# Optimization experiments

Measured on AMD Instinct MI355X. Metric: run time of the kernel, lower is better.

The kernel has to match this reference:

```python
import jax, jax.numpy as jnp
import numpy as np

B, H, S, D = 2, 12, 3456, 32
FEATS_PER_T = 216
WINDOW_LEN = 8
ACT_SIZE = 16
IMG_FEAT_SIZE = 196
DECODER_ONLY = False


def eye_mask(seq_len, feats_per_t, window_len, act_size, img_feat_size, decoder_only=False):
    """Boolean [S, S] mask replicating get_eye_block_mask's memory_mask."""
    idx = jnp.arange(seq_len)
    q_t = (idx // feats_per_t)[:, None]          # [S,1]
    kv_t = (idx // feats_per_t)[None, :]         # [1,S]
    q_m = (idx % feats_per_t)[:, None]
    kv_m = (idx % feats_per_t)[None, :]
    proprio_idx_mod = 2 + 1 + 1
    img_start = feats_per_t - img_feat_size
    joint_start = img_start - act_size

    causal = (q_t >= kv_t) & (q_t - kv_t < window_len)
    is_q_img = q_m >= img_start
    is_kv_img = kv_m >= img_start
    is_q_joint = (q_m >= joint_start) & (q_m < img_start)
    is_kv_joint = (kv_m >= joint_start) & (kv_m < img_start)
    is_kv_proprio = kv_m == proprio_idx_mod

    img_to_img = ~(is_q_img & is_kv_img)
    same_t = q_t == kv_t
    joint_past_joint = ~(is_q_joint & is_kv_joint & ~same_t)
    proprio_past = ~(is_kv_proprio & (kv_t < q_t))
    past_image = ~(is_kv_img & (kv_t < q_t))
    m = causal & img_to_img & joint_past_joint & proprio_past & past_image
    if decoder_only:
        m = m & ~(is_q_img & ~is_kv_img)
    return m


def setup_inputs() -> dict:
    key = jax.random.key(0)
    kq, kk, kv = jax.random.split(key, 3)
    return {
        "q": jax.random.normal(kq, (B, H, S, D), dtype=jnp.float32),
        "k": jax.random.normal(kk, (B, H, S, D), dtype=jnp.float32),
        "v": jax.random.normal(kv, (B, H, S, D), dtype=jnp.float32),
        "feats_per_t": FEATS_PER_T,
        "window_len": WINDOW_LEN,
        "act_size": ACT_SIZE,
        "img_feat_size": IMG_FEAT_SIZE,
    }


def reference(q, k, v, feats_per_t, window_len, act_size, img_feat_size):
    seq_len = q.shape[2]
    mask = eye_mask(seq_len, feats_per_t, window_len, act_size,
                    img_feat_size, DECODER_ONLY)  # [S,S]
    scale = 1.0 / jnp.sqrt(jnp.array(q.shape[-1], q.dtype))
    scores = jnp.einsum("bhqd,bhkd->bhqk", q, k) * scale
    neg = jnp.asarray(jnp.finfo(scores.dtype).min, scores.dtype)
    scores = jnp.where(mask[None, None], scores, neg)
    attn = jax.nn.softmax(scores, axis=-1)
    return jnp.einsum("bhqk,bhkd->bhqd", attn, v)
```

## Files before the change

### kernel.cpp

```cpp
#include <hip/hip_runtime.h>

#define SEQ   3456
#define DH    32
#define FPT   216
#define NT    16
#define IMG0  20
#define SCALE2 0.25503486f

#define KPAD   40
#define VPAD   168
#define PPITCH 36

typedef __attribute__((ext_vector_type(8))) short bf16x8;
typedef __attribute__((ext_vector_type(4))) short bf16x4;
typedef __attribute__((ext_vector_type(4))) float f32x4;

#define MFMA16(a,b,c) __builtin_amdgcn_mfma_f32_16x16x32_bf16(a,b,c,0,0,0)

__device__ __forceinline__ unsigned short bfh(float f) {
    unsigned u = __float_as_uint(f);
    u += 0x7FFFu + ((u >> 16) & 1u);
    return (unsigned short)(u >> 16);
}
__device__ __forceinline__ float bff(unsigned short h) {
    return __uint_as_float((unsigned)h << 16);
}
__device__ __forceinline__ void split8(const float* f, bf16x8& hi, bf16x8& lo) {
    #pragma unroll
    for (int j = 0; j < 8; ++j) {
        unsigned short h = bfh(f[j]);
        hi[j] = (short)h;
        lo[j] = (short)bfh(f[j] - bff(h));
    }
}
__device__ __forceinline__ bf16x8 load_p(const unsigned short* p) {
    const bf16x4 a = *(const bf16x4*)(p);
    const bf16x4 b = *(const bf16x4*)(p + 4);
    bf16x8 r;
    #pragma unroll
    for (int j = 0; j < 4; ++j) { r[j] = a[j]; r[4 + j] = b[j]; }
    return r;
}

__global__ __launch_bounds__(256, 4)
void eye_attn_mfma2(const float* __restrict__ q, const float* __restrict__ k,
                    const float* __restrict__ v, float* __restrict__ out) {
    __shared__ __align__(16) unsigned short KsHi[160 * KPAD];
    __shared__ __align__(16) unsigned short KsLo[160 * KPAD];
    __shared__ __align__(16) unsigned short VtHi[DH * VPAD];
    __shared__ __align__(16) unsigned short Pu[4 * 16 * PPITCH];

    const int t = blockIdx.x, bh = blockIdx.y, half = blockIdx.z;
    const int tid = threadIdx.x;
    const size_t base = (size_t)bh * SEQ * DH;
    const int dmax = (t < 7) ? t : 7;
    const int nkeys = IMG0 * (dmax + 1);

    for (int i = tid; i < 160 * 8; i += 256) {
        const int g = i >> 3, c = i & 7;
        float4 kk = make_float4(0.f,0.f,0.f,0.f), vv = make_float4(0.f,0.f,0.f,0.f);
        if (g < nkeys) {
            const int d = g / IMG0, jj = g - d * IMG0;
            const size_t row = base + (size_t)((t - d) * FPT + jj) * DH + c * 4;
            kk = *(const float4*)(k + row);
            vv = *(const float4*)(v + row);
        }
        const float kf[4] = {kk.x, kk.y, kk.z, kk.w};
        const float vf[4] = {vv.x, vv.y, vv.z, vv.w};
        ushort4 khi, klo;
        unsigned short* ah = (unsigned short*)&khi;
        unsigned short* al = (unsigned short*)&klo;
        #pragma unroll
        for (int e = 0; e < 4; ++e) {
            const unsigned short h = bfh(kf[e]);
            ah[e] = h;
            al[e] = bfh(kf[e] - bff(h));
        }
        *(ushort4*)(KsHi + g * KPAD + c * 4) = khi;
        *(ushort4*)(KsLo + g * KPAD + c * 4) = klo;
        #pragma unroll
        for (int e = 0; e < 4; ++e)
            VtHi[(c * 4 + e) * VPAD + g] = bfh(vf[e]);
    }
    __syncthreads();

    const int wv = tid >> 6, lane = tid & 63;
    const int col = lane & 15, quad = lane >> 4;

    int mt[2]; int mcnt; bool do_img = false;
    if (half == 0) {
        if (wv == 0)      { mt[0] = 0; mcnt = 1; do_img = true; }
        else if (wv == 1) { mt[0] = 1; mcnt = 1; do_img = true; }
        else if (wv == 2) { mt[0] = 2; mt[1] = 3; mcnt = 2; }
        else              { mt[0] = 4; mt[1] = 5; mcnt = 2; }
    } else {
        mt[0] = 6 + 2 * wv; mt[1] = 7 + 2 * wv; mcnt = 2;
    }

    bf16x8 bones;
    #pragma unroll
    for (int j = 0; j < 8; ++j) bones[j] = (short)(col == 0 ? 0x3F80 : 0);

    unsigned short* myP = Pu + wv * 16 * PPITCH;
    const int nkt = (nkeys + 31) >> 5;

    for (int mi = 0; mi < mcnt; ++mi) {
        const int mb = mt[mi] * 16;
        bf16x8 qhi, qlo;
        {
            const int qc = min(mb + col, FPT - 1);
            const float* qp = q + base + (size_t)(t * FPT + qc) * DH + quad * 8;
            float qf[8];
            const float4 a0 = *(const float4*)qp;
            const float4 a1 = *(const float4*)(qp + 4);
            qf[0]=a0.x*SCALE2; qf[1]=a0.y*SCALE2; qf[2]=a0.z*SCALE2; qf[3]=a0.w*SCALE2;
            qf[4]=a1.x*SCALE2; qf[5]=a1.y*SCALE2; qf[6]=a1.z*SCALE2; qf[7]=a1.w*SCALE2;
            split8(qf, qhi, qlo);
        }
        f32x4 oacc0 = {0.f,0.f,0.f,0.f}, oacc1 = {0.f,0.f,0.f,0.f};
        f32x4 lacc = {0.f,0.f,0.f,0.f};

        for (int kt = 0; kt < nkt; ++kt) {
            f32x4 s[2];
            #pragma unroll
            for (int h = 0; h < 2; ++h) {
                const int key = kt * 32 + h * 16 + col;
                const bf16x8 khi = *(const bf16x8*)(KsHi + key * KPAD + quad * 8);
                const bf16x8 klo = *(const bf16x8*)(KsLo + key * KPAD + quad * 8);
                f32x4 acc = {0.f,0.f,0.f,0.f};
                acc = MFMA16(qhi, khi, acc);
                acc = MFMA16(qlo, khi, acc);
                acc = MFMA16(qhi, klo, acc);
                s[h] = acc;
            }
            #pragma unroll
            for (int h = 0; h < 2; ++h) {
                const int g = kt * 32 + h * 16 + col;
                const int d = g / IMG0, jj = g - d * IMG0;
                #pragma unroll
                for (int r = 0; r < 4; ++r) {
                    const int qm = mb + quad * 4 + r;
                    const bool qj = (qm >= 4) && (qm < IMG0);
                    const bool vis = (g < nkeys) && (qm < FPT) &&
                                     ((d == 0) || ((jj != 4) && !(qj && jj >= 4)));
                    const float e = vis ? __builtin_amdgcn_exp2f(s[h][r]) : 0.f;
                    myP[(quad * 4 + r) * PPITCH + h * 16 + col] = bfh(e);
                }
            }
            const bf16x8 phi = load_p(myP + col * PPITCH + quad * 8);
            #pragma unroll
            for (int h = 0; h < 2; ++h) {
                const int dim = h * 16 + col;
                const bf16x8 vhi = *(const bf16x8*)(VtHi + dim * VPAD + kt * 32 + quad * 8);
                f32x4& oa = h ? oacc1 : oacc0;
                oa = MFMA16(phi, vhi, oa);
            }
            lacc = MFMA16(phi, bones, lacc);
        }

        if (mi == 0 && do_img) {
            for (int kt2 = 0; kt2 < 7; ++kt2) {
                f32x4 s[2];
                #pragma unroll
                for (int h = 0; h < 2; ++h) {
                    const int keyc = min(IMG0 + kt2 * 32 + h * 16 + col, FPT - 1);
                    const float* kp = k + base + (size_t)(t * FPT + keyc) * DH + quad * 8;
                    float kf[8];
                    const float4 a0 = *(const float4*)kp;
                    const float4 a1 = *(const float4*)(kp + 4);
                    kf[0]=a0.x; kf[1]=a0.y; kf[2]=a0.z; kf[3]=a0.w;
                    kf[4]=a1.x; kf[5]=a1.y; kf[6]=a1.z; kf[7]=a1.w;
                    bf16x8 khi, klo;
                    split8(kf, khi, klo);
                    f32x4 acc = {0.f,0.f,0.f,0.f};
                    acc = MFMA16(qhi, khi, acc);
                    acc = MFMA16(qlo, khi, acc);
                    acc = MFMA16(qhi, klo, acc);
                    s[h] = acc;
                }
                #pragma unroll
                for (int h = 0; h < 2; ++h) {
                    const int key = IMG0 + kt2 * 32 + h * 16 + col;
                    #pragma unroll
                    for (int r = 0; r < 4; ++r) {
                        const int qm = mb + quad * 4 + r;
                        const bool vis = (key < FPT) && (qm < IMG0);
                        const float e = vis ? __builtin_amdgcn_exp2f(s[h][r]) : 0.f;
                        myP[(quad * 4 + r) * PPITCH + h * 16 + col] = bfh(e);
                    }
                }
                const bf16x8 phi = load_p(myP + col * PPITCH + quad * 8);
                #pragma unroll
                for (int h = 0; h < 2; ++h) {
                    const int dim = h * 16 + col;
                    float vf[8];
                    #pragma unroll
                    for (int j = 0; j < 8; ++j) {
                        const int ky = min(IMG0 + kt2 * 32 + quad * 8 + j, FPT - 1);
                        vf[j] = v[base + (size_t)(t * FPT + ky) * DH + dim];
                    }
                    bf16x8 vhi;
                    #pragma unroll
                    for (int j = 0; j < 8; ++j) vhi[j] = (short)bfh(vf[j]);
                    f32x4& oa = h ? oacc1 : oacc0;
                    oa = MFMA16(phi, vhi, oa);
                }
                lacc = MFMA16(phi, bones, lacc);
            }
        }

        #pragma unroll
        for (int r = 0; r < 4; ++r) {
            const float lr = __shfl(lacc[r], lane & 48);
            const float inv = 1.f / lr;
            const int qm = mb + quad * 4 + r;
            if (qm < FPT) {
                float* op = out + base + (size_t)(t * FPT + qm) * DH;
                op[col]      = oacc0[r] * inv;
                op[16 + col] = oacc1[r] * inv;
            }
        }
    }
}

extern "C" void kernel_launch(void* const* d_in, const int* in_sizes, int n_in,
                              void* d_out, int out_size, void* d_ws, size_t ws_size,
                              hipStream_t stream) {
    const float* q = (const float*)d_in[0];
    const float* k = (const float*)d_in[1];
    const float* v = (const float*)d_in[2];
    float* out = (float*)d_out;
    const int BH = in_sizes[0] / (SEQ * DH);
    dim3 grid(NT, BH, 2);
    eye_attn_mfma2<<<grid, 256, 0, stream>>>(q, k, v, out);
}
```

Measured before the change: 97.11 us.

## Compute transposed scores so P stays in registers as MFMA B operand

Swaps the MFMA operand order so the score tile is produced transposed (keys along rows, queries along columns). Each lane's exp'd probabilities can then feed the P·V MFMA directly as the B operand, which removes the per-wave LDS round-trip for P and its shared buffer. The V tile is read with two 64-bit LDS loads in the matching permuted key order, and VPAD changes. The row sum now uses an all-ones A operand, and the output is written as float4 vectors without a shuffle.

```diff
diff --git a/kernel.cpp b/kernel.cpp
--- a/kernel.cpp
+++ b/kernel.cpp
@@ -8,8 +8,7 @@
 #define SCALE2 0.25503486f
 
 #define KPAD   40
-#define VPAD   168
-#define PPITCH 36
+#define VPAD   164
 
 typedef __attribute__((ext_vector_type(8))) short bf16x8;
 typedef __attribute__((ext_vector_type(4))) short bf16x4;
@@ -33,9 +32,9 @@
         lo[j] = (short)bfh(f[j] - bff(h));
     }
 }
-__device__ __forceinline__ bf16x8 load_p(const unsigned short* p) {
-    const bf16x4 a = *(const bf16x4*)(p);
-    const bf16x4 b = *(const bf16x4*)(p + 4);
+__device__ __forceinline__ bf16x8 ld2x64(const unsigned short* p0, const unsigned short* p1) {
+    const bf16x4 a = *(const bf16x4*)p0;
+    const bf16x4 b = *(const bf16x4*)p1;
     bf16x8 r;
     #pragma unroll
     for (int j = 0; j < 4; ++j) { r[j] = a[j]; r[4 + j] = b[j]; }
@@ -43,12 +42,11 @@
 }
 
 __global__ __launch_bounds__(256, 4)
-void eye_attn_mfma2(const float* __restrict__ q, const float* __restrict__ k,
+void eye_attn_mfma3(const float* __restrict__ q, const float* __restrict__ k,
                     const float* __restrict__ v, float* __restrict__ out) {
     __shared__ __align__(16) unsigned short KsHi[160 * KPAD];
     __shared__ __align__(16) unsigned short KsLo[160 * KPAD];
     __shared__ __align__(16) unsigned short VtHi[DH * VPAD];
-    __shared__ __align__(16) unsigned short Pu[4 * 16 * PPITCH];
 
     const int t = blockIdx.x, bh = blockIdx.y, half = blockIdx.z;
     const int tid = threadIdx.x;
@@ -97,18 +95,21 @@
         mt[0] = 6 + 2 * wv; mt[1] = 7 + 2 * wv; mcnt = 2;
     }
 
-    bf16x8 bones;
+    bf16x8 ones8;
     #pragma unroll
-    for (int j = 0; j < 8; ++j) bones[j] = (short)(col == 0 ? 0x3F80 : 0);
-
-    unsigned short* myP = Pu + wv * 16 * PPITCH;
+    for (int j = 0; j < 8; ++j) ones8[j] = (short)0x3F80;
+
     const int nkt = (nkeys + 31) >> 5;
+    const int gq = quad * 4;
 
     for (int mi = 0; mi < mcnt; ++mi) {
         const int mb = mt[mi] * 16;
+        const int qm = mb + col;
+        const bool qok = qm < FPT;
+        const bool qj  = (qm >= 4) && (qm < IMG0);
         bf16x8 qhi, qlo;
         {
-            const int qc = min(mb + col, FPT - 1);
+            const int qc = min(qm, FPT - 1);
             const float* qp = q + base + (size_t)(t * FPT + qc) * DH + quad * 8;
             float qf[8];
             const float4 a0 = *(const float4*)qp;
@@ -128,34 +129,32 @@
                 const bf16x8 khi = *(const bf16x8*)(KsHi + key * KPAD + quad * 8);
                 const bf16x8 klo = *(const bf16x8*)(KsLo + key * KPAD + quad * 8);
                 f32x4 acc = {0.f,0.f,0.f,0.f};
-                acc = MFMA16(qhi, khi, acc);
-                acc = MFMA16(qlo, khi, acc);
-                acc = MFMA16(qhi, klo, acc);
+                acc = MFMA16(khi, qhi, acc);
+                acc = MFMA16(khi, qlo, acc);
+                acc = MFMA16(klo, qhi, acc);
                 s[h] = acc;
             }
+            bf16x8 pb;
             #pragma unroll
             for (int h = 0; h < 2; ++h) {
-                const int g = kt * 32 + h * 16 + col;
-                const int d = g / IMG0, jj = g - d * IMG0;
                 #pragma unroll
                 for (int r = 0; r < 4; ++r) {
-                    const int qm = mb + quad * 4 + r;
-                    const bool qj = (qm >= 4) && (qm < IMG0);
-                    const bool vis = (g < nkeys) && (qm < FPT) &&
+                    const int g = kt * 32 + h * 16 + gq + r;
+                    const int d = g / IMG0, jj = g - d * IMG0;
+                    const bool vis = (g < nkeys) && qok &&
                                      ((d == 0) || ((jj != 4) && !(qj && jj >= 4)));
                     const float e = vis ? __builtin_amdgcn_exp2f(s[h][r]) : 0.f;
-                    myP[(quad * 4 + r) * PPITCH + h * 16 + col] = bfh(e);
-                }
-            }
-            const bf16x8 phi = load_p(myP + col * PPITCH + quad * 8);
+                    pb[h * 4 + r] = (short)bfh(e);
+                }
+            }
+            lacc = MFMA16(ones8, pb, lacc);
             #pragma unroll
-            for (int h = 0; h < 2; ++h) {
-                const int dim = h * 16 + col;
-                const bf16x8 vhi = *(const bf16x8*)(VtHi + dim * VPAD + kt * 32 + quad * 8);
-                f32x4& oa = h ? oacc1 : oacc0;
-                oa = MFMA16(phi, vhi, oa);
-            }
-            lacc = MFMA16(phi, bones, lacc);
+            for (int h2 = 0; h2 < 2; ++h2) {
+                const unsigned short* vp = VtHi + (h2 * 16 + col) * VPAD + kt * 32 + quad * 4;
+                const bf16x8 va = ld2x64(vp, vp + 16);
+                f32x4& oa = h2 ? oacc1 : oacc0;
+                oa = MFMA16(va, pb, oa);
+            }
         }
 
         if (mi == 0 && do_img) {
@@ -173,52 +172,48 @@
                     bf16x8 khi, klo;
                     split8(kf, khi, klo);
                     f32x4 acc = {0.f,0.f,0.f,0.f};
-                    acc = MFMA16(qhi, khi, acc);
-                    acc = MFMA16(qlo, khi, acc);
-                    acc = MFMA16(qhi, klo, acc);
+                    acc = MFMA16(khi, qhi, acc);
+                    acc = MFMA16(khi, qlo, acc);
+                    acc = MFMA16(klo, qhi, acc);
                     s[h] = acc;
                 }
+                bf16x8 pb;
                 #pragma unroll
                 for (int h = 0; h < 2; ++h) {
-                    const int key = IMG0 + kt2 * 32 + h * 16 + col;
                     #pragma unroll
                     for (int r = 0; r < 4; ++r) {
-                        const int qm = mb + quad * 4 + r;
+                        const int key = IMG0 + kt2 * 32 + h * 16 + gq + r;
                         const bool vis = (key < FPT) && (qm < IMG0);
                         const float e = vis ? __builtin_amdgcn_exp2f(s[h][r]) : 0.f;
-                        myP[(quad * 4 + r) * PPITCH + h * 16 + col] = bfh(e);
+                        pb[h * 4 + r] = (short)bfh(e);
                     }
                 }
-                const bf16x8 phi = load_p(myP + col * PPITCH + quad * 8);
-                #pragma unroll
-                for (int h = 0; h < 2; ++h) {
-                    const int dim = h * 16 + col;
+                lacc = MFMA16(ones8, pb, lacc);
+                #pragma unroll
+                for (int h2 = 0; h2 < 2; ++h2) {
                     float vf[8];
                     #pragma unroll
                     for (int j = 0; j < 8; ++j) {
-                        const int ky = min(IMG0 + kt2 * 32 + quad * 8 + j, FPT - 1);
-                        vf[j] = v[base + (size_t)(t * FPT + ky) * DH + dim];
+                        const int ky = min(IMG0 + kt2 * 32 + 16 * (j >> 2) + gq + (j & 3), FPT - 1);
+                        vf[j] = v[base + (size_t)(t * FPT + ky) * DH + h2 * 16 + col];
                     }
-                    bf16x8 vhi;
+                    bf16x8 va;
                     #pragma unroll
-                    for (int j = 0; j < 8; ++j) vhi[j] = (short)bfh(vf[j]);
-                    f32x4& oa = h ? oacc1 : oacc0;
-                    oa = MFMA16(phi, vhi, oa);
-                }
-                lacc = MFMA16(phi, bones, lacc);
-            }
-        }
-
-        #pragma unroll
-        for (int r = 0; r < 4; ++r) {
-            const float lr = __shfl(lacc[r], lane & 48);
-            const float inv = 1.f / lr;
-            const int qm = mb + quad * 4 + r;
-            if (qm < FPT) {
-                float* op = out + base + (size_t)(t * FPT + qm) * DH;
-                op[col]      = oacc0[r] * inv;
-                op[16 + col] = oacc1[r] * inv;
-            }
+                    for (int j = 0; j < 8; ++j) va[j] = (short)bfh(vf[j]);
+                    f32x4& oa = h2 ? oacc1 : oacc0;
+                    oa = MFMA16(va, pb, oa);
+                }
+            }
+        }
+
+        if (qok) {
+            const float inv = 1.f / lacc[0];
+            float* op = out + base + (size_t)(t * FPT + qm) * DH;
+            float4 o0, o1;
+            o0.x = oacc0[0]*inv; o0.y = oacc0[1]*inv; o0.z = oacc0[2]*inv; o0.w = oacc0[3]*inv;
+            o1.x = oacc1[0]*inv; o1.y = oacc1[1]*inv; o1.z = oacc1[2]*inv; o1.w = oacc1[3]*inv;
+            *(float4*)(op + quad * 4)      = o0;
+            *(float4*)(op + 16 + quad * 4) = o1;
         }
     }
 }
@@ -232,5 +227,5 @@
     float* out = (float*)d_out;
     const int BH = in_sizes[0] / (SEQ * DH);
     dim3 grid(NT, BH, 2);
-    eye_attn_mfma2<<<grid, 256, 0, stream>>>(q, k, v, out);
-}
+    eye_attn_mfma3<<<grid, 256, 0, stream>>>(q, k, v, out);
+}
```

Result: no change. 97.35 us (+0.3%).
